# Performance work log

Measured on AMD Instinct MI355X. Metric: run time of the kernel, lower is better.

Reference implementation:

```python
import jax, jax.numpy as jnp
import numpy as np

N_NODES = 100000
N_EDGES = 1600000
GENE_DIM = 256
HID = 128
NUM_CLASSES = 2
BN_EPS = 1e-5


def setup_inputs() -> dict:
    key = jax.random.key(0)
    ks = jax.random.split(key, 24)
    g = lambda k, shape, scale: (jax.random.normal(k, shape, dtype=jnp.float32) * scale)
    inp = {
        "x": g(ks[0], (N_NODES, GENE_DIM), 1.0),
        "edge_index": jax.random.randint(ks[1], (2, N_EDGES), 0, N_NODES, dtype=jnp.int64),
        # GCNConv weights (glorot-ish scale) and biases
        "W1": g(ks[2], (GENE_DIM, HID), 1.0 / np.sqrt(GENE_DIM)), "b1": jnp.zeros((HID,), jnp.float32),
        "W2": g(ks[3], (HID, 2 * HID), 1.0 / np.sqrt(HID)), "b2": jnp.zeros((2 * HID,), jnp.float32),
        "W3": g(ks[4], (2 * HID, HID), 1.0 / np.sqrt(2 * HID)), "b3": jnp.zeros((HID,), jnp.float32),
        "W4": g(ks[5], (HID, HID // 2), 1.0 / np.sqrt(HID)), "b4": jnp.zeros((HID // 2,), jnp.float32),
        "Wc": g(ks[6], (HID // 2, NUM_CLASSES), 1.0 / np.sqrt(HID // 2)), "bc": jnp.zeros((NUM_CLASSES,), jnp.float32),
        # BatchNorm affine params
        "g1": jnp.ones((HID,), jnp.float32), "be1": jnp.zeros((HID,), jnp.float32),
        "g2": jnp.ones((2 * HID,), jnp.float32), "be2": jnp.zeros((2 * HID,), jnp.float32),
        "g3": jnp.ones((HID,), jnp.float32), "be3": jnp.zeros((HID,), jnp.float32),
        "g4": jnp.ones((HID // 2,), jnp.float32), "be4": jnp.zeros((HID // 2,), jnp.float32),
    }
    return inp


def _batchnorm(h, gamma, beta):
    # training-mode BatchNorm1d: per-feature batch stats (biased variance)
    mean = h.mean(axis=0)
    var = ((h - mean) ** 2).mean(axis=0)
    return gamma * (h - mean) * jax.lax.rsqrt(var + BN_EPS) + beta


def _gcn_conv(h, W, b, src, dst, norm, n):
    # PyG GCNConv: linear transform, then sym-normalized aggregation over
    # edges (self-loops already included in src/dst/norm), then bias.
    m = h @ W                                   # [n, d_out]
    msg = m[src] * norm[:, None]                # [E+n, d_out] gather
    agg = jax.ops.segment_sum(msg, dst, num_segments=n)  # scatter-add
    return agg + b


def reference(x, edge_index, W1, b1, W2, b2, W3, b3, W4, b4, Wc, bc,
              g1, be1, g2, be2, g3, be3, g4, be4):
    n = x.shape[0]
    loop = jnp.arange(n, dtype=edge_index.dtype)
    src = jnp.concatenate([edge_index[0], loop])  # add self-loops
    dst = jnp.concatenate([edge_index[1], loop])
    deg = jax.ops.segment_sum(jnp.ones_like(dst, dtype=x.dtype), dst, num_segments=n)
    dinv = jax.lax.rsqrt(jnp.maximum(deg, 1.0))
    norm = dinv[src] * dinv[dst]                  # D^-1/2 (A+I) D^-1/2

    h = jax.nn.relu(_gcn_conv(x, W1, b1, src, dst, norm, n))
    h = _batchnorm(h, g1, be1)
    h = jax.nn.relu(_gcn_conv(h, W2, b2, src, dst, norm, n))
    h = _batchnorm(h, g2, be2)
    h = jax.nn.relu(_gcn_conv(h, W3, b3, src, dst, norm, n))
    h = _batchnorm(h, g3, be3)
    out4 = jax.nn.relu(_gcn_conv(h, W4, b4, src, dst, norm, n))
    bn4 = _batchnorm(out4, g4, be4)
    logits = bn4 @ Wc + bc
    return (logits, out4, bn4)
```

## Files before the change

kernel.cpp:

```cpp
#include <hip/hip_runtime.h>
#include <hip/hip_bf16.h>

#define N_NODES 100000
#define N_EDGES 1600000
#define NB ((N_NODES + 255) / 256)
#define CHUNK 16384
#define NBLK ((N_EDGES + CHUNK - 1) / CHUNK)
#define NSHADOW 64

typedef short sh8 __attribute__((ext_vector_type(8)));
typedef float f32x4 __attribute__((ext_vector_type(4)));

__device__ __forceinline__ float bf2f(unsigned short s) {
    return __uint_as_float(((unsigned int)s) << 16);
}
__device__ __forceinline__ unsigned short f2bf(float f) {
    unsigned int u = __float_as_uint(f);
    unsigned int r = (u + 0x7FFFu + ((u >> 16) & 1u)) >> 16;
    return (unsigned short)r;
}
__device__ __forceinline__ float blo(unsigned int u) { return __uint_as_float(u << 16); }
__device__ __forceinline__ float bhi(unsigned int u) { return __uint_as_float(u & 0xffff0000u); }


__global__ __launch_bounds__(256) void k_hist(const int* __restrict__ ei, int* __restrict__ histG) {
    __shared__ int hist[NB];
    int blk = blockIdx.x, t = threadIdx.x;
    for (int b = t; b < NB; b += 256) hist[b] = 0;
    __syncthreads();
    int e0 = blk * CHUNK;
    int e1 = min(e0 + CHUNK, N_EDGES);
    for (int e = e0 + t; e < e1; e += 256) atomicAdd(&hist[ei[N_EDGES + e] >> 8], 1);
    __syncthreads();
    for (int b = t; b < NB; b += 256) histG[b * NBLK + blk] = hist[b];
}

__global__ __launch_bounds__(128) void k_scanrow(int* __restrict__ histG, int* __restrict__ rowsum) {
    __shared__ int sm[128];
    int b = blockIdx.x, t = threadIdx.x;
    int v = (t < NBLK) ? histG[b * NBLK + t] : 0;
    sm[t] = v; __syncthreads();
    for (int d = 1; d < 128; d <<= 1) {
        int add = (t >= d) ? sm[t - d] : 0;
        __syncthreads(); sm[t] += add; __syncthreads();
    }
    if (t < NBLK) histG[b * NBLK + t] = sm[t] - v;
    if (t == 127) rowsum[b] = sm[127];
}

__global__ __launch_bounds__(512) void k_scanbkt(const int* __restrict__ rowsum, int* __restrict__ rowbase) {
    __shared__ int sm[512];
    int t = threadIdx.x;
    int v = (t < NB) ? rowsum[t] : 0;
    sm[t] = v; __syncthreads();
    for (int d = 1; d < 512; d <<= 1) {
        int add = (t >= d) ? sm[t - d] : 0;
        __syncthreads(); sm[t] += add; __syncthreads();
    }
    if (t <= NB) rowbase[t] = sm[t] - v;
}

__global__ __launch_bounds__(256) void k_part(const int* __restrict__ ei, const int* __restrict__ histG,
                                              const int* __restrict__ rowbase, unsigned* __restrict__ pairs) {
    __shared__ int cur[NB];
    int blk = blockIdx.x, t = threadIdx.x;
    for (int b = t; b < NB; b += 256) cur[b] = rowbase[b] + histG[b * NBLK + blk];
    __syncthreads();
    int e0 = blk * CHUNK;
    int e1 = min(e0 + CHUNK, N_EDGES);
    for (int e = e0 + t; e < e1; e += 256) {
        int s = ei[e], d = ei[N_EDGES + e];
        int pos = atomicAdd(&cur[d >> 8], 1);
        pairs[pos] = ((unsigned)s << 8) | (unsigned)(d & 255);
    }
}

__global__ __launch_bounds__(256) void k_bsort(const unsigned* __restrict__ pairs, const int* __restrict__ rowbase,
                                               int* __restrict__ col, int* __restrict__ basep,
                                               int* __restrict__ deg, float* __restrict__ dinv,
                                               float* __restrict__ sdeg) {
    __shared__ int cnt[256];
    __shared__ int sm[256];
    __shared__ int cur[256];
    int b = blockIdx.x, t = threadIdx.x;
    int base = rowbase[b], end = rowbase[b + 1];
    cnt[t] = 0; __syncthreads();
    for (int e = base + t; e < end; e += 256) atomicAdd(&cnt[pairs[e] & 255], 1);
    __syncthreads();
    int v = cnt[t];
    sm[t] = v; __syncthreads();
    for (int d = 1; d < 256; d <<= 1) {
        int add = (t >= d) ? sm[t - d] : 0;
        __syncthreads(); sm[t] += add; __syncthreads();
    }
    int excl = sm[t] - v;
    cur[t] = excl;
    int gd = (b << 8) + t;
    if (gd < N_NODES) {
        basep[gd] = base + excl;
        deg[gd] = v;
        dinv[gd] = rsqrtf((float)(v + 1));
        sdeg[gd] = sqrtf((float)(v + 1));
    }
    __syncthreads();
    for (int e = base + t; e < end; e += 256) {
        unsigned p = pairs[e];
        int pos = atomicAdd(&cur[p & 255], 1);
        col[base + pos] = (int)(p >> 8);
    }
}

__global__ __launch_bounds__(256) void k_svec(const int* __restrict__ col, const int* __restrict__ basep,
                                              const int* __restrict__ deg, const float* __restrict__ dinv,
                                              float* __restrict__ svec) {
    int w = (blockIdx.x * 256 + threadIdx.x) >> 6;
    if (w >= N_NODES) return;
    int lane = threadIdx.x & 63;
    int start = basep[w], cnt = deg[w];
    float s = 0.f;
    for (int j = lane; j < cnt; j += 64) s += dinv[col[start + j]];
#pragma unroll
    for (int off = 32; off; off >>= 1) s += __shfl_down(s, off, 64);
    if (lane == 0) { float di = dinv[w]; svec[w] = di * (s + di); }
}


__global__ void k_wconv_all(const float* __restrict__ W1, const float* __restrict__ W2,
                            const float* __restrict__ W3, const float* __restrict__ W4,
                            unsigned short* __restrict__ Wt1, unsigned short* __restrict__ Wt2,
                            unsigned short* __restrict__ Wt3, unsigned short* __restrict__ Wt4) {
    int idx = blockIdx.x * 256 + threadIdx.x;
    const float* W; unsigned short* Wt; int K, N, base;
    if (idx < 32768)       { W = W1; Wt = Wt1; K = 256; N = 128; base = 0; }
    else if (idx < 65536)  { W = W2; Wt = Wt2; K = 128; N = 256; base = 32768; }
    else if (idx < 98304)  { W = W3; Wt = Wt3; K = 256; N = 128; base = 65536; }
    else if (idx < 106496) { W = W4; Wt = Wt4; K = 128; N = 64;  base = 98304; }
    else return;
    int li = idx - base;
    int n = li / K, k = li - n * K;
    Wt[li] = f2bf(W[(size_t)k * N + n]);
}


__global__ __launch_bounds__(256) void k_bnred(float* __restrict__ shadow, float* __restrict__ dst) {
    int f = blockIdx.x * 256 + threadIdx.x;
    float s = 0.f;
#pragma unroll
    for (int i = 0; i < NSHADOW; ++i) {
        s += shadow[i * 512 + f];
        shadow[i * 512 + f] = 0.f;
    }
    dst[f] = s;
}


template <int D, bool INF32, bool RESCALE>
__global__ __launch_bounds__(256) void k_bnstats(const void* __restrict__ h,
                                                 const float* __restrict__ sdeg,
                                                 float* __restrict__ shadow) {
    constexpr int VEC = INF32 ? 4 : 8;
    constexpr int TPR = D / VEC;
    constexpr int RPB = 256 / TPR;
    const int tid = threadIdx.x;
    const int rg = tid / TPR;
    const int oc = tid % TPR;
    const int fb = oc * VEC;

    float s1[VEC], s2[VEC];
#pragma unroll
    for (int k = 0; k < VEC; ++k) { s1[k] = 0.f; s2[k] = 0.f; }

    for (int r = blockIdx.x * RPB + rg; r < N_NODES; r += gridDim.x * RPB) {
        float rs = 1.f;
        if constexpr (RESCALE) rs = sdeg[r];
        if constexpr (INF32) {
            float4 v = *(const float4*)((const float*)h + (size_t)r * D + fb);
            float vv[4] = {v.x, v.y, v.z, v.w};
#pragma unroll
            for (int k = 0; k < 4; ++k) {
                float val = vv[k];
                if constexpr (RESCALE) val *= rs;
                s1[k] += val; s2[k] += val * val;
            }
        } else {
            uint4 u = *(const uint4*)((const unsigned short*)h + (size_t)r * D + fb);
            unsigned uu[4] = {u.x, u.y, u.z, u.w};
#pragma unroll
            for (int k = 0; k < 4; ++k) {
                float v0 = blo(uu[k]), v1 = bhi(uu[k]);
                if constexpr (RESCALE) { v0 *= rs; v1 *= rs; }
                s1[2 * k] += v0;     s2[2 * k] += v0 * v0;
                s1[2 * k + 1] += v1; s2[2 * k + 1] += v1 * v1;
            }
        }
    }

    __shared__ float red[2][D];
    for (int i = tid; i < 2 * D; i += 256) ((float*)red)[i] = 0.f;
    __syncthreads();
#pragma unroll
    for (int k = 0; k < VEC; ++k) {
        atomicAdd(&red[0][fb + k], s1[k]);
        atomicAdd(&red[1][fb + k], s2[k]);
    }
    __syncthreads();
    float* slot = shadow + ((blockIdx.x & (NSHADOW - 1)) << 9);
    for (int i = tid; i < 2 * D; i += 256) {
        int f = (i < D) ? i : (256 + i - D);
        float v = (i < D) ? red[0][i] : red[1][i - D];
        atomicAdd(&slot[f], v);
    }
}


template <int BN, int NWM, int NWN, int AMODE, bool BIASRELU, bool DSCALE>
__global__ __launch_bounds__(256) void k_gemm2(const void* __restrict__ Ain,
                                               const unsigned short* __restrict__ Wt,
                                               const float* __restrict__ sums_in,
                                               const float* __restrict__ gamma,
                                               const float* __restrict__ beta,
                                               const float* __restrict__ svec,
                                               const float* __restrict__ bias,
                                               const float* __restrict__ dinv,
                                               unsigned short* __restrict__ Mout,
                                               int K, int NTOT) {
    constexpr int BK = 64;
    constexpr int LDA = 72;
    constexpr int MF = 64 / (16 * NWM);
    constexpr int NF = BN / (16 * NWN);
    constexpr int BP = BN / 32;
    __shared__ unsigned short As[64 * LDA];
    __shared__ unsigned short Bs[BN * LDA];
    __shared__ float ss_sc[256];
    __shared__ float ss_sh[256];
    const int tid = threadIdx.x;
    const int lane = tid & 63;
    const int w = tid >> 6;
    const int wm = w / NWN, wn = w % NWN;
    const int row0 = blockIdx.x * 64;
    const int col0 = blockIdx.y * BN;

    if constexpr (AMODE >= 1) {
        for (int f = tid; f < K; f += 256) {
            float mean = sums_in[f] * (1.f / N_NODES);
            float var = sums_in[256 + f] * (1.f / N_NODES) - mean * mean;
            float inv = rsqrtf(var + 1e-5f);
            float sc = gamma[f] * inv;
            ss_sc[f] = sc;
            ss_sh[f] = beta[f] - mean * sc;
        }
        __syncthreads();
    }

    const int sr = tid >> 3;
    const int scc = (tid & 7) * 8;

    float4 fa[2][2];
    uint4 ua[2];
    uint4 ub[BP];
    float sv[2];

    auto LOAD = [&](int k0) {
        if constexpr (AMODE == 0) {
            const float* Af = (const float*)Ain;
#pragma unroll
            for (int p = 0; p < 2; ++p) {
                int gr = row0 + p * 32 + sr;
                fa[p][0] = make_float4(0.f, 0.f, 0.f, 0.f); fa[p][1] = fa[p][0];
                if (gr < N_NODES) {
                    const float* p0 = Af + (size_t)gr * K + k0 + scc;
                    fa[p][0] = *(const float4*)p0;
                    fa[p][1] = *(const float4*)(p0 + 4);
                }
            }
        } else {
            const unsigned short* Ab = (const unsigned short*)Ain;
#pragma unroll
            for (int p = 0; p < 2; ++p) {
                int gr = row0 + p * 32 + sr;
                ua[p] = make_uint4(0, 0, 0, 0);
                if (gr < N_NODES) ua[p] = *(const uint4*)(Ab + (size_t)gr * K + k0 + scc);
                if constexpr (AMODE == 2) sv[p] = (gr < N_NODES) ? svec[gr] : 0.f;
            }
        }
#pragma unroll
        for (int p = 0; p < BP; ++p) {
            int r = p * 32 + sr;
            ub[p] = *(const uint4*)(Wt + (size_t)(col0 + r) * K + k0 + scc);
        }
    };

    auto WRITE = [&](int k0) {
#pragma unroll
        for (int p = 0; p < 2; ++p) {
            alignas(16) unsigned short tmp[8];
            if constexpr (AMODE == 0) {
                tmp[0] = f2bf(fa[p][0].x); tmp[1] = f2bf(fa[p][0].y);
                tmp[2] = f2bf(fa[p][0].z); tmp[3] = f2bf(fa[p][0].w);
                tmp[4] = f2bf(fa[p][1].x); tmp[5] = f2bf(fa[p][1].y);
                tmp[6] = f2bf(fa[p][1].z); tmp[7] = f2bf(fa[p][1].w);
            } else {
                const unsigned short* pr = (const unsigned short*)&ua[p];
#pragma unroll
                for (int q = 0; q < 8; ++q) {
                    float sc = ss_sc[k0 + scc + q];
                    float sh = ss_sh[k0 + scc + q];
                    float val;
                    if constexpr (AMODE == 2) val = bf2f(pr[q]) * sc + sh * sv[p];
                    else val = bf2f(pr[q]) * sc + sh;
                    tmp[q] = f2bf(val);
                }
            }
            *(uint4*)&As[(p * 32 + sr) * LDA + scc] = *(const uint4*)tmp;
        }
#pragma unroll
        for (int p = 0; p < BP; ++p) *(uint4*)&Bs[(p * 32 + sr) * LDA + scc] = ub[p];
    };

    f32x4 acc[MF][NF];
#pragma unroll
    for (int i = 0; i < MF; ++i)
#pragma unroll
        for (int j = 0; j < NF; ++j)
#pragma unroll
            for (int r = 0; r < 4; ++r) acc[i][j][r] = 0.f;

    LOAD(0);
    WRITE(0);
    __syncthreads();
    const int nk = K / BK;
    for (int kt = 1; kt <= nk; ++kt) {
        if (kt < nk) LOAD(kt * BK);
#pragma unroll
        for (int ks = 0; ks < 2; ++ks) {
            sh8 af[MF], bfr[NF];
#pragma unroll
            for (int i = 0; i < MF; ++i)
                af[i] = *(const sh8*)&As[(wm * MF * 16 + i * 16 + (lane & 15)) * LDA + ks * 32 + (lane >> 4) * 8];
#pragma unroll
            for (int j = 0; j < NF; ++j)
                bfr[j] = *(const sh8*)&Bs[(wn * NF * 16 + j * 16 + (lane & 15)) * LDA + ks * 32 + (lane >> 4) * 8];
#pragma unroll
            for (int i = 0; i < MF; ++i)
#pragma unroll
                for (int j = 0; j < NF; ++j)
                    acc[i][j] = __builtin_amdgcn_mfma_f32_16x16x32_bf16(af[i], bfr[j], acc[i][j], 0, 0, 0);
        }
        __syncthreads();
        if (kt < nk) {
            WRITE(kt * BK);
            __syncthreads();
        }
    }

#pragma unroll
    for (int i = 0; i < MF; ++i) {
#pragma unroll
        for (int r = 0; r < 4; ++r) {
            int grow = row0 + wm * MF * 16 + i * 16 + (lane >> 4) * 4 + r;
            if (grow >= N_NODES) continue;
            float rsc = 1.f;
            if constexpr (DSCALE) rsc = dinv[grow];
#pragma unroll
            for (int j = 0; j < NF; ++j) {
                int gcol = col0 + wn * NF * 16 + j * 16 + (lane & 15);
                float v = acc[i][j][r];
                if constexpr (BIASRELU) v = fmaxf(v + bias[gcol], 0.f);
                if constexpr (DSCALE) v *= rsc;
                Mout[(size_t)grow * NTOT + gcol] = f2bf(v);
            }
        }
    }
}


template <int D, bool PRE, bool OUTF32, bool OUTSCALE>
__global__ __launch_bounds__(256) void k_agg(const unsigned short* __restrict__ m,
                                             const int* __restrict__ col,
                                             const int* __restrict__ basep,
                                             const int* __restrict__ deg,
                                             const float* __restrict__ dinv,
                                             const float* __restrict__ bias,
                                             void* __restrict__ out) {
    constexpr int VPL = D / 64;
    const int w = (blockIdx.x * 256 + threadIdx.x) >> 6;
    if (w >= N_NODES) return;
    const int lane = threadIdx.x & 63;
    const int fo = lane * VPL;
    const unsigned short* mfo = m + fo;
    float acc[VPL];
#pragma unroll
    for (int k = 0; k < VPL; ++k) acc[k] = 0.f;

    int start = basep[w], cnt = deg[w];
    int j = 0;
    for (; j + 8 <= cnt; j += 8) {
        int sx[8];
#pragma unroll
        for (int i = 0; i < 8; ++i) sx[i] = col[start + j + i];
        if constexpr (VPL == 2) {
            unsigned u[8];
#pragma unroll
            for (int i = 0; i < 8; ++i) u[i] = *(const unsigned*)(mfo + (size_t)sx[i] * D);
#pragma unroll
            for (int i = 0; i < 8; ++i) { acc[0] += blo(u[i]); acc[1] += bhi(u[i]); }
        } else {
            float v[8];
#pragma unroll
            for (int i = 0; i < 8; ++i) v[i] = bf2f(mfo[(size_t)sx[i] * D]);
#pragma unroll
            for (int i = 0; i < 8; ++i) acc[0] += v[i];
        }
    }
    for (; j < cnt; ++j) {
        int s0 = col[start + j];
        if constexpr (VPL == 2) {
            unsigned u0 = *(const unsigned*)(mfo + (size_t)s0 * D);
            acc[0] += blo(u0); acc[1] += bhi(u0);
        } else {
            acc[0] += bf2f(mfo[(size_t)s0 * D]);
        }
    }
    if constexpr (VPL == 2) {
        unsigned u0 = *(const unsigned*)(mfo + (size_t)w * D);
        acc[0] += blo(u0); acc[1] += bhi(u0);
    } else {
        acc[0] += bf2f(mfo[(size_t)w * D]);
    }

    float di = dinv[w];
    float o[VPL];
    if constexpr (PRE) {
#pragma unroll
        for (int k = 0; k < VPL; ++k) o[k] = acc[k] * di;
    } else {
#pragma unroll
        for (int k = 0; k < VPL; ++k) {
            o[k] = fmaxf(acc[k] * di + bias[fo + k], 0.f);
            if constexpr (OUTSCALE) o[k] *= di;
        }
    }

    if constexpr (OUTF32) {
        float* of = (float*)out;
#pragma unroll
        for (int k = 0; k < VPL; ++k) of[(size_t)w * D + fo + k] = o[k];
    } else {
        unsigned short* ob = (unsigned short*)out + (size_t)w * D + fo;
        if constexpr (VPL == 2) {
            unsigned int u = (unsigned)f2bf(o[0]) | ((unsigned)f2bf(o[1]) << 16);
            *(unsigned int*)ob = u;
        } else {
            ob[0] = f2bf(o[0]);
        }
    }
}


__global__ __launch_bounds__(256) void k_bnlog(const float* __restrict__ out4, const float* __restrict__ sums,
                                               const float* __restrict__ gamma, const float* __restrict__ beta,
                                               const float* __restrict__ Wc, const float* __restrict__ bc,
                                               float* __restrict__ bn4, float* __restrict__ logits) {
    int gw = (blockIdx.x * 256 + threadIdx.x) >> 6;
    if (gw >= N_NODES) return;
    int f = threadIdx.x & 63;
    float mean = sums[f] * (1.f / N_NODES);
    float var = sums[256 + f] * (1.f / N_NODES) - mean * mean;
    float inv = rsqrtf(var + 1e-5f);
    float sc = gamma[f] * inv;
    float sh = beta[f] - mean * sc;
    float v = out4[(size_t)gw * 64 + f];
    float bn = v * sc + sh;
    bn4[(size_t)gw * 64 + f] = bn;
    float a0 = bn * Wc[2 * f];
    float a1 = bn * Wc[2 * f + 1];
#pragma unroll
    for (int off = 32; off; off >>= 1) {
        a0 += __shfl_down(a0, off, 64);
        a1 += __shfl_down(a1, off, 64);
    }
    if (f == 0) {
        logits[2 * gw] = a0 + bc[0];
        logits[2 * gw + 1] = a1 + bc[1];
    }
}


extern "C" void kernel_launch(void* const* d_in, const int* in_sizes, int n_in,
                              void* d_out, int out_size, void* d_ws, size_t ws_size,
                              hipStream_t stream) {
    const float* x  = (const float*)d_in[0];
    const int* ei   = (const int*)d_in[1];
    const float* W1 = (const float*)d_in[2];  const float* b1  = (const float*)d_in[3];
    const float* W2 = (const float*)d_in[4];  const float* b2  = (const float*)d_in[5];
    const float* W3 = (const float*)d_in[6];  const float* b3  = (const float*)d_in[7];
    const float* W4 = (const float*)d_in[8];  const float* b4  = (const float*)d_in[9];
    const float* Wc = (const float*)d_in[10]; const float* bc  = (const float*)d_in[11];
    const float* g1 = (const float*)d_in[12]; const float* be1 = (const float*)d_in[13];
    const float* g2 = (const float*)d_in[14]; const float* be2 = (const float*)d_in[15];
    const float* g3 = (const float*)d_in[16]; const float* be3 = (const float*)d_in[17];
    const float* g4 = (const float*)d_in[18]; const float* be4 = (const float*)d_in[19];

    char* wsb = (char*)d_ws;
    size_t off = 0;
    auto alloc = [&](size_t bytes) -> void* {
        void* p = wsb + off;
        off = (off + bytes + 511) & ~(size_t)511;
        return p;
    };
    int* deg     = (int*)alloc((size_t)N_NODES * 4);
    int* basep   = (int*)alloc((size_t)N_NODES * 4);
    float* dinv  = (float*)alloc((size_t)N_NODES * 4);
    float* sdeg  = (float*)alloc((size_t)N_NODES * 4);
    float* svec  = (float*)alloc((size_t)N_NODES * 4);
    int* col     = (int*)alloc((size_t)N_EDGES * 4);
    unsigned* pairs = (unsigned*)alloc((size_t)N_EDGES * 4);
    int* histG   = (int*)alloc((size_t)NB * NBLK * 4);
    int* rowsum  = (int*)alloc((size_t)NB * 4);
    int* rowbase = (int*)alloc((size_t)(NB + 1) * 4);
    float* sums  = (float*)alloc(2048 * 4);
    float* shadow = (float*)alloc((size_t)NSHADOW * 512 * 4);
    unsigned short* Wt1 = (unsigned short*)alloc((size_t)256 * 128 * 2);
    unsigned short* Wt2 = (unsigned short*)alloc((size_t)128 * 256 * 2);
    unsigned short* Wt3 = (unsigned short*)alloc((size_t)256 * 128 * 2);
    unsigned short* Wt4 = (unsigned short*)alloc((size_t)128 * 64 * 2);
    unsigned short* mb = (unsigned short*)alloc((size_t)N_NODES * 128 * 2);
    unsigned short* hb = (unsigned short*)alloc((size_t)N_NODES * 256 * 2);

    float* sums1 = sums, *sums2 = sums + 512, *sums3 = sums + 1024, *sums4 = sums + 1536;

    float* outLogits = (float*)d_out;
    float* out4 = outLogits + (size_t)N_NODES * 2;
    float* bn4  = out4 + (size_t)N_NODES * 64;

    hipMemsetAsync(sums, 0, 2048 * 4, stream);
    hipMemsetAsync(shadow, 0, (size_t)NSHADOW * 512 * 4, stream);

    k_hist<<<NBLK, 256, 0, stream>>>(ei, histG);
    k_scanrow<<<NB, 128, 0, stream>>>(histG, rowsum);
    k_scanbkt<<<1, 512, 0, stream>>>(rowsum, rowbase);
    k_part<<<NBLK, 256, 0, stream>>>(ei, histG, rowbase, pairs);
    k_bsort<<<NB, 256, 0, stream>>>(pairs, rowbase, col, basep, deg, dinv, sdeg);
    k_svec<<<(N_NODES + 3) / 4, 256, 0, stream>>>(col, basep, deg, dinv, svec);

    k_wconv_all<<<(106496 + 255) / 256, 256, 0, stream>>>(W1, W2, W3, W4, Wt1, Wt2, Wt3, Wt4);

    const int GBM = (N_NODES + 63) / 64;
    const int AB = (N_NODES + 3) / 4;
    const int SB = 512;

    k_gemm2<128, 1, 4, 0, false, true><<<dim3(GBM, 1), 256, 0, stream>>>(
        x, Wt1, nullptr, nullptr, nullptr, nullptr, nullptr, dinv, mb, 256, 128);
    k_agg<128, false, false, true><<<AB, 256, 0, stream>>>(
        mb, col, basep, deg, dinv, b1, hb);
    k_bnstats<128, false, true><<<SB, 256, 0, stream>>>(hb, sdeg, shadow);
    k_bnred<<<2, 256, 0, stream>>>(shadow, sums1);

    k_agg<128, true, false, false><<<AB, 256, 0, stream>>>(
        hb, col, basep, deg, dinv, nullptr, mb);
    k_gemm2<128, 1, 4, 2, true, false><<<dim3(GBM, 2), 256, 0, stream>>>(
        mb, Wt2, sums1, g1, be1, svec, b2, nullptr, hb, 128, 256);
    k_bnstats<256, false, false><<<SB, 256, 0, stream>>>(hb, nullptr, shadow);
    k_bnred<<<2, 256, 0, stream>>>(shadow, sums2);

    k_gemm2<128, 1, 4, 1, false, true><<<dim3(GBM, 1), 256, 0, stream>>>(
        hb, Wt3, sums2, g2, be2, nullptr, nullptr, dinv, mb, 256, 128);
    k_agg<128, false, false, false><<<AB, 256, 0, stream>>>(
        mb, col, basep, deg, dinv, b3, hb);
    k_bnstats<128, false, false><<<SB, 256, 0, stream>>>(hb, nullptr, shadow);
    k_bnred<<<2, 256, 0, stream>>>(shadow, sums3);

    k_gemm2<64, 2, 2, 1, false, true><<<dim3(GBM, 1), 256, 0, stream>>>(
        hb, Wt4, sums3, g3, be3, nullptr, nullptr, dinv, mb, 128, 64);
    k_agg<64, false, true, false><<<AB, 256, 0, stream>>>(
        mb, col, basep, deg, dinv, b4, out4);
    k_bnstats<64, true, false><<<SB, 256, 0, stream>>>(out4, nullptr, shadow);
    k_bnred<<<2, 256, 0, stream>>>(shadow, sums4);
    k_bnlog<<<(N_NODES * 64 + 255) / 256, 256, 0, stream>>>(out4, sums4, g4, be4, Wc, bc, bn4, outLogits);
}
```

Baseline: 660.4 us.

## Use 512-thread GEMM blocks and batch neighbor gathers by 16 in aggregation

The GEMM kernel moves from 256 to 512 threads per 64-row tile, using 8 waves in a 2x4 arrangement. Each thread now loads one A row slice and fewer B rows, which lowers per-thread register pressure and adds waves available to hide latency. The aggregation kernel replaces its 8-wide unrolled loop, scalar tail and separate self-loop load with a single loop over 16-wide batches. Out-of-range slots in a batch are clamped to the node itself and masked out of the sum, so more gathers are in flight at once at the cost of some wasted loads on low-degree nodes.

```diff
diff --git a/kernel.cpp b/kernel.cpp
--- a/kernel.cpp
+++ b/kernel.cpp
@@ -213,8 +213,8 @@
 }
 
 
-template <int BN, int NWM, int NWN, int AMODE, bool BIASRELU, bool DSCALE>
-__global__ __launch_bounds__(256) void k_gemm2(const void* __restrict__ Ain,
+template <int BN, int AMODE, bool BIASRELU, bool DSCALE>
+__global__ __launch_bounds__(512) void k_gemm3(const void* __restrict__ Ain,
                                                const unsigned short* __restrict__ Wt,
                                                const float* __restrict__ sums_in,
                                                const float* __restrict__ gamma,
@@ -226,22 +226,23 @@
                                                int K, int NTOT) {
     constexpr int BK = 64;
     constexpr int LDA = 72;
-    constexpr int MF = 64 / (16 * NWM);
-    constexpr int NF = BN / (16 * NWN);
-    constexpr int BP = BN / 32;
+    constexpr int MF = 2;
+    constexpr int NF = BN / 64;
+    constexpr int BP = BN / 64;
     __shared__ unsigned short As[64 * LDA];
     __shared__ unsigned short Bs[BN * LDA];
     __shared__ float ss_sc[256];
     __shared__ float ss_sh[256];
     const int tid = threadIdx.x;
     const int lane = tid & 63;
-    const int w = tid >> 6;
-    const int wm = w / NWN, wn = w % NWN;
+    const int wv = tid >> 6;
+    const int wm = wv >> 2;
+    const int wn = wv & 3;
     const int row0 = blockIdx.x * 64;
     const int col0 = blockIdx.y * BN;
 
     if constexpr (AMODE >= 1) {
-        for (int f = tid; f < K; f += 256) {
+        for (int f = tid; f < K; f += 512) {
             float mean = sums_in[f] * (1.f / N_NODES);
             float var = sums_in[256 + f] * (1.f / N_NODES) - mean * mean;
             float inv = rsqrtf(var + 1e-5f);
@@ -255,66 +256,54 @@
     const int sr = tid >> 3;
     const int scc = (tid & 7) * 8;
 
-    float4 fa[2][2];
-    uint4 ua[2];
+    float4 fa[2];
+    uint4 ua;
     uint4 ub[BP];
-    float sv[2];
+    float sv = 0.f;
 
     auto LOAD = [&](int k0) {
+        int gr = row0 + sr;
         if constexpr (AMODE == 0) {
             const float* Af = (const float*)Ain;
-#pragma unroll
-            for (int p = 0; p < 2; ++p) {
-                int gr = row0 + p * 32 + sr;
-                fa[p][0] = make_float4(0.f, 0.f, 0.f, 0.f); fa[p][1] = fa[p][0];
-                if (gr < N_NODES) {
-                    const float* p0 = Af + (size_t)gr * K + k0 + scc;
-                    fa[p][0] = *(const float4*)p0;
-                    fa[p][1] = *(const float4*)(p0 + 4);
-                }
+            fa[0] = make_float4(0.f, 0.f, 0.f, 0.f); fa[1] = fa[0];
+            if (gr < N_NODES) {
+                const float* p0 = Af + (size_t)gr * K + k0 + scc;
+                fa[0] = *(const float4*)p0;
+                fa[1] = *(const float4*)(p0 + 4);
             }
         } else {
             const unsigned short* Ab = (const unsigned short*)Ain;
-#pragma unroll
-            for (int p = 0; p < 2; ++p) {
-                int gr = row0 + p * 32 + sr;
-                ua[p] = make_uint4(0, 0, 0, 0);
-                if (gr < N_NODES) ua[p] = *(const uint4*)(Ab + (size_t)gr * K + k0 + scc);
-                if constexpr (AMODE == 2) sv[p] = (gr < N_NODES) ? svec[gr] : 0.f;
-            }
-        }
-#pragma unroll
-        for (int p = 0; p < BP; ++p) {
-            int r = p * 32 + sr;
-            ub[p] = *(const uint4*)(Wt + (size_t)(col0 + r) * K + k0 + scc);
-        }
+            ua = make_uint4(0, 0, 0, 0);
+            if (gr < N_NODES) ua = *(const uint4*)(Ab + (size_t)gr * K + k0 + scc);
+            if constexpr (AMODE == 2) sv = (gr < N_NODES) ? svec[gr] : 0.f;
+        }
+#pragma unroll
+        for (int p = 0; p < BP; ++p)
+            ub[p] = *(const uint4*)(Wt + (size_t)(col0 + p * 64 + sr) * K + k0 + scc);
     };
 
     auto WRITE = [&](int k0) {
-#pragma unroll
-        for (int p = 0; p < 2; ++p) {
-            alignas(16) unsigned short tmp[8];
-            if constexpr (AMODE == 0) {
-                tmp[0] = f2bf(fa[p][0].x); tmp[1] = f2bf(fa[p][0].y);
-                tmp[2] = f2bf(fa[p][0].z); tmp[3] = f2bf(fa[p][0].w);
-                tmp[4] = f2bf(fa[p][1].x); tmp[5] = f2bf(fa[p][1].y);
-                tmp[6] = f2bf(fa[p][1].z); tmp[7] = f2bf(fa[p][1].w);
-            } else {
-                const unsigned short* pr = (const unsigned short*)&ua[p];
-#pragma unroll
-                for (int q = 0; q < 8; ++q) {
-                    float sc = ss_sc[k0 + scc + q];
-                    float sh = ss_sh[k0 + scc + q];
-                    float val;
-                    if constexpr (AMODE == 2) val = bf2f(pr[q]) * sc + sh * sv[p];
-                    else val = bf2f(pr[q]) * sc + sh;
-                    tmp[q] = f2bf(val);
-                }
-            }
-            *(uint4*)&As[(p * 32 + sr) * LDA + scc] = *(const uint4*)tmp;
-        }
-#pragma unroll
-        for (int p = 0; p < BP; ++p) *(uint4*)&Bs[(p * 32 + sr) * LDA + scc] = ub[p];
+        alignas(16) unsigned short tmp[8];
+        if constexpr (AMODE == 0) {
+            tmp[0] = f2bf(fa[0].x); tmp[1] = f2bf(fa[0].y);
+            tmp[2] = f2bf(fa[0].z); tmp[3] = f2bf(fa[0].w);
+            tmp[4] = f2bf(fa[1].x); tmp[5] = f2bf(fa[1].y);
+            tmp[6] = f2bf(fa[1].z); tmp[7] = f2bf(fa[1].w);
+        } else {
+            const unsigned short* pr = (const unsigned short*)&ua;
+#pragma unroll
+            for (int q = 0; q < 8; ++q) {
+                float sc = ss_sc[k0 + scc + q];
+                float sh = ss_sh[k0 + scc + q];
+                float val;
+                if constexpr (AMODE == 2) val = bf2f(pr[q]) * sc + sh * sv;
+                else val = bf2f(pr[q]) * sc + sh;
+                tmp[q] = f2bf(val);
+            }
+        }
+        *(uint4*)&As[sr * LDA + scc] = *(const uint4*)tmp;
+#pragma unroll
+        for (int p = 0; p < BP; ++p) *(uint4*)&Bs[(p * 64 + sr) * LDA + scc] = ub[p];
     };
 
     f32x4 acc[MF][NF];
@@ -336,7 +325,7 @@
             sh8 af[MF], bfr[NF];
 #pragma unroll
             for (int i = 0; i < MF; ++i)
-                af[i] = *(const sh8*)&As[(wm * MF * 16 + i * 16 + (lane & 15)) * LDA + ks * 32 + (lane >> 4) * 8];
+                af[i] = *(const sh8*)&As[(wm * 32 + i * 16 + (lane & 15)) * LDA + ks * 32 + (lane >> 4) * 8];
 #pragma unroll
             for (int j = 0; j < NF; ++j)
                 bfr[j] = *(const sh8*)&Bs[(wn * NF * 16 + j * 16 + (lane & 15)) * LDA + ks * 32 + (lane >> 4) * 8];
@@ -357,7 +346,7 @@
     for (int i = 0; i < MF; ++i) {
 #pragma unroll
         for (int r = 0; r < 4; ++r) {
-            int grow = row0 + wm * MF * 16 + i * 16 + (lane >> 4) * 4 + r;
+            int grow = row0 + wm * 32 + i * 16 + (lane >> 4) * 4 + r;
             if (grow >= N_NODES) continue;
             float rsc = 1.f;
             if constexpr (DSCALE) rsc = dinv[grow];
@@ -383,6 +372,7 @@
                                              const float* __restrict__ bias,
                                              void* __restrict__ out) {
     constexpr int VPL = D / 64;
+    constexpr int BT = 16;
     const int w = (blockIdx.x * 256 + threadIdx.x) >> 6;
     if (w >= N_NODES) return;
     const int lane = threadIdx.x & 63;
@@ -392,40 +382,37 @@
 #pragma unroll
     for (int k = 0; k < VPL; ++k) acc[k] = 0.f;
 
-    int start = basep[w], cnt = deg[w];
-    int j = 0;
-    for (; j + 8 <= cnt; j += 8) {
-        int sx[8];
-#pragma unroll
-        for (int i = 0; i < 8; ++i) sx[i] = col[start + j + i];
+    const int start = basep[w];
+    const int cnt = deg[w];
+    const int total = cnt + 1;
+
+    for (int j = 0; j < total; j += BT) {
+        int sx[BT];
+#pragma unroll
+        for (int i = 0; i < BT; ++i) {
+            int idx = j + i;
+            int ca = start + idx;
+            ca = (ca < N_EDGES) ? ca : (N_EDGES - 1);
+            int c = col[ca];
+            sx[i] = (idx < cnt) ? c : w;
+        }
         if constexpr (VPL == 2) {
-            unsigned u[8];
-#pragma unroll
-            for (int i = 0; i < 8; ++i) u[i] = *(const unsigned*)(mfo + (size_t)sx[i] * D);
-#pragma unroll
-            for (int i = 0; i < 8; ++i) { acc[0] += blo(u[i]); acc[1] += bhi(u[i]); }
+            unsigned u[BT];
+#pragma unroll
+            for (int i = 0; i < BT; ++i) u[i] = *(const unsigned*)(mfo + (size_t)sx[i] * D);
+#pragma unroll
+            for (int i = 0; i < BT; ++i) {
+                if (j + i < total) { acc[0] += blo(u[i]); acc[1] += bhi(u[i]); }
+            }
         } else {
-            float v[8];
-#pragma unroll
-            for (int i = 0; i < 8; ++i) v[i] = bf2f(mfo[(size_t)sx[i] * D]);
-#pragma unroll
-            for (int i = 0; i < 8; ++i) acc[0] += v[i];
-        }
-    }
-    for (; j < cnt; ++j) {
-        int s0 = col[start + j];
-        if constexpr (VPL == 2) {
-            unsigned u0 = *(const unsigned*)(mfo + (size_t)s0 * D);
-            acc[0] += blo(u0); acc[1] += bhi(u0);
-        } else {
-            acc[0] += bf2f(mfo[(size_t)s0 * D]);
-        }
-    }
-    if constexpr (VPL == 2) {
-        unsigned u0 = *(const unsigned*)(mfo + (size_t)w * D);
-        acc[0] += blo(u0); acc[1] += bhi(u0);
-    } else {
-        acc[0] += bf2f(mfo[(size_t)w * D]);
+            unsigned short us[BT];
+#pragma unroll
+            for (int i = 0; i < BT; ++i) us[i] = mfo[(size_t)sx[i] * D];
+#pragma unroll
+            for (int i = 0; i < BT; ++i) {
+                if (j + i < total) acc[0] += bf2f(us[i]);
+            }
+        }
     }
 
     float di = dinv[w];
@@ -549,7 +536,7 @@
     const int AB = (N_NODES + 3) / 4;
     const int SB = 512;
 
-    k_gemm2<128, 1, 4, 0, false, true><<<dim3(GBM, 1), 256, 0, stream>>>(
+    k_gemm3<128, 0, false, true><<<dim3(GBM, 1), 512, 0, stream>>>(
         x, Wt1, nullptr, nullptr, nullptr, nullptr, nullptr, dinv, mb, 256, 128);
     k_agg<128, false, false, true><<<AB, 256, 0, stream>>>(
         mb, col, basep, deg, dinv, b1, hb);
@@ -558,19 +545,19 @@
 
     k_agg<128, true, false, false><<<AB, 256, 0, stream>>>(
         hb, col, basep, deg, dinv, nullptr, mb);
-    k_gemm2<128, 1, 4, 2, true, false><<<dim3(GBM, 2), 256, 0, stream>>>(
+    k_gemm3<128, 2, true, false><<<dim3(GBM, 2), 512, 0, stream>>>(
         mb, Wt2, sums1, g1, be1, svec, b2, nullptr, hb, 128, 256);
     k_bnstats<256, false, false><<<SB, 256, 0, stream>>>(hb, nullptr, shadow);
     k_bnred<<<2, 256, 0, stream>>>(shadow, sums2);
 
-    k_gemm2<128, 1, 4, 1, false, true><<<dim3(GBM, 1), 256, 0, stream>>>(
+    k_gemm3<128, 1, false, true><<<dim3(GBM, 1), 512, 0, stream>>>(
         hb, Wt3, sums2, g2, be2, nullptr, nullptr, dinv, mb, 256, 128);
     k_agg<128, false, false, false><<<AB, 256, 0, stream>>>(
         mb, col, basep, deg, dinv, b3, hb);
     k_bnstats<128, false, false><<<SB, 256, 0, stream>>>(hb, nullptr, shadow);
     k_bnred<<<2, 256, 0, stream>>>(shadow, sums3);
 
-    k_gemm2<64, 2, 2, 1, false, true><<<dim3(GBM, 1), 256, 0, stream>>>(
+    k_gemm3<64, 1, false, true><<<dim3(GBM, 1), 512, 0, stream>>>(
         hb, Wt4, sums3, g3, be3, nullptr, nullptr, dinv, mb, 128, 64);
     k_agg<64, false, true, false><<<AB, 256, 0, stream>>>(
         mb, col, basep, deg, dinv, b4, out4);
```

Measured after the change: 653.1 us. About the same (-1.1%).
